# Kernel optimization log

Measured on AMD Instinct MI355X. Metric: run time of the kernel, lower is better.

## Reference

```python
import jax, jax.numpy as jnp
import numpy as np
jax.config.update('jax_enable_x64', True)

B, S, D, H, V, P = 4, 2048, 512, 8, 100000, 256
NGRAMS = list(range(3, 9))  # n-gram lengths 3..8
DH = D // H
SCALE = np.float32(DH ** -0.5)

def _layernorm(x, g, b, eps=1e-5):
    m = jnp.mean(x, -1, keepdims=True)
    v = jnp.mean(jnp.square(x - m), -1, keepdims=True)
    return g * (x - m) / jnp.sqrt(v + eps) + b

def _mha(q, k, v, Wq, bq, Wk, bk, Wv, bv, Wo, bo):
    Bq, Lq, _ = q.shape
    qh = (q @ Wq + bq).reshape(Bq, Lq, H, DH)
    kh = (k @ Wk + bk).reshape(Bq, -1, H, DH)
    vh = (v @ Wv + bv).reshape(Bq, -1, H, DH)
    s = jnp.einsum('bqhd,bkhd->bhqk', qh, kh) * SCALE
    a = jax.nn.softmax(s, axis=-1)
    o = jnp.einsum('bhqk,bkhd->bqhd', a, vh).reshape(Bq, Lq, D)
    return o @ Wo + bo

def _ngram_hash(bytes_seq, n):
    # hash[:, i] = sum_k bytes[:, i-n+1+k] * 256**k for i >= n-1 else 0, then mod V
    # (int64 wraparound for n=8 matches torch semantics)
    b = bytes_seq.astype(jnp.int64)
    h = jnp.zeros_like(b)
    for k in range(n):
        shift = n - 1 - k
        shifted = jnp.pad(b, ((0, 0), (shift, 0)))[:, :S]
        h = h + shifted * (256 ** k)
    h = jnp.where(jnp.arange(S) >= (n - 1), h, 0)
    return h % V

def _forward(bytes_seq, patch_idx, byte_emb, ngram_emb, sWq, sbq, sWk, sbk, sWv, sbv, sWo, sbo, ln1g, ln1b, W1, b1, W2, b2, ln2g, ln2b, cWq, cbq, cWk, cbk, cWv, cbv, cWo, cbo):
    embeds = byte_emb[bytes_seq]  # [B,S,D]
    for j, n in enumerate(NGRAMS):
        embeds = embeds + ngram_emb[j][_ngram_hash(bytes_seq, n)]
    embeds = embeds / np.float32(len(NGRAMS) + 1)
    # one post-norm transformer encoder layer (relu FFN, eval mode / no dropout)
    x = _layernorm(embeds + _mha(embeds, embeds, embeds, sWq, sbq, sWk, sbk, sWv, sbv, sWo, sbo), ln1g, ln1b)
    ff = jax.nn.relu(x @ W1 + b1) @ W2 + b2
    x = _layernorm(x + ff, ln2g, ln2b)
    # gather patch-boundary queries per batch, cross-attend to full sequence
    q = jnp.take_along_axis(x, patch_idx[..., None], axis=1)  # [B,P,D]
    return _mha(q, x, x, cWq, cbq, cWk, cbk, cWv, cbv, cWo, cbo)

def setup_inputs():
    key = jax.random.key(0)
    ks = jax.random.split(key, 20)
    f32 = jnp.float32
    def rn(k, shape, scale=0.02):
        return (jax.random.normal(k, shape, f32) * scale).astype(f32)
    return {
        'bytes_seq': jax.random.randint(ks[0], (B, S), 0, 256, dtype=jnp.int64),
        'patch_idx': jnp.sort(jax.random.randint(ks[1], (B, P), 0, S, dtype=jnp.int64), axis=1),
        'byte_emb': rn(ks[2], (256, D)),
        'ngram_emb': rn(ks[3], (len(NGRAMS), V, D)),
        'sWq': rn(ks[4], (D, D)), 'sbq': jnp.zeros((D,), f32),
        'sWk': rn(ks[5], (D, D)), 'sbk': jnp.zeros((D,), f32),
        'sWv': rn(ks[6], (D, D)), 'sbv': jnp.zeros((D,), f32),
        'sWo': rn(ks[7], (D, D)), 'sbo': jnp.zeros((D,), f32),
        'ln1g': jnp.ones((D,), f32), 'ln1b': jnp.zeros((D,), f32),
        'W1': rn(ks[8], (D, 4 * D)), 'b1': jnp.zeros((4 * D,), f32),
        'W2': rn(ks[9], (4 * D, D)), 'b2': jnp.zeros((D,), f32),
        'ln2g': jnp.ones((D,), f32), 'ln2b': jnp.zeros((D,), f32),
        'cWq': rn(ks[10], (D, D)), 'cbq': jnp.zeros((D,), f32),
        'cWk': rn(ks[11], (D, D)), 'cbk': jnp.zeros((D,), f32),
        'cWv': rn(ks[12], (D, D)), 'cbv': jnp.zeros((D,), f32),
        'cWo': rn(ks[13], (D, D)), 'cbo': jnp.zeros((D,), f32),
    }

def reference(bytes_seq, patch_idx, byte_emb, ngram_emb, sWq, sbq, sWk, sbk, sWv, sbv, sWo, sbo, ln1g, ln1b, W1, b1, W2, b2, ln2g, ln2b, cWq, cbq, cWk, cbk, cWv, cbv, cWo, cbo):
    return _forward(bytes_seq, patch_idx, byte_emb, ngram_emb, sWq, sbq, sWk, sbk, sWv, sbv, sWo, sbo, ln1g, ln1b, W1, b1, W2, b2, ln2g, ln2b, cWq, cbq, cWk, cbk, cWv, cbv, cWo, cbo)
```

## Files before the change

kernel.cpp:

```cpp
#include <hip/hip_runtime.h>
#include <stdint.h>

#define B_   4
#define S_   2048
#define D_   512
#define H_   8
#define DH_  64
#define V_   100000
#define P_   256
#define N_   (B_*S_)
#define NP_  (B_*P_)

typedef _Float16 f16;
typedef _Float16 f16x8 __attribute__((ext_vector_type(8)));
typedef float    f32x4 __attribute__((ext_vector_type(4)));
typedef uint32_t u32x4 __attribute__((ext_vector_type(4)));

#define MFMA16(a,b,c) __builtin_amdgcn_mfma_f32_16x16x32_f16((a),(b),(c),0,0,0)
#define GLDS16(gp, lp) __builtin_amdgcn_global_load_lds( \
    (const __attribute__((address_space(1))) void*)(gp), \
    (__attribute__((address_space(3))) void*)(lp), 16, 0, 0)

struct WJobs {
  const float* src[10];
  f16* dst[10];
  int K[10], N[10], tiles[10];
};

__global__ __launch_bounds__(256) void prep_kernel(WJobs jobs,
    const float* __restrict__ sbq, const float* __restrict__ sbk,
    const float* __restrict__ sbv, const float* __restrict__ cbk,
    const float* __restrict__ cbv, float* __restrict__ bqkv,
    float* __restrict__ bckv,
    const int* __restrict__ bytes_seq, const float* __restrict__ byte_emb,
    const float* __restrict__ ngram_emb, f16* __restrict__ out16)
{
  int bid = blockIdx.x;
  if (bid < 10240) {
    const int j = bid >> 10, tile = bid & 1023;
    if (tile >= jobs.tiles[j]) return;
    const int K = jobs.K[j], N = jobs.N[j];
    const int ntiles = N >> 5;
    const int kt = (tile / ntiles) << 5, nt = (tile % ntiles) << 5;
    __shared__ float T[32][33];
    const int t = threadIdx.x;
    const float* src = jobs.src[j];
    #pragma unroll
    for (int p = 0; p < 4; p++) {
      int lin = t + p * 256;
      int rr = lin >> 5, cc = lin & 31;
      T[rr][cc] = src[(size_t)(kt + rr) * N + nt + cc];
    }
    __syncthreads();
    f16* dst = jobs.dst[j];
    #pragma unroll
    for (int p = 0; p < 4; p++) {
      int lin = t + p * 256;
      int rr = lin >> 5, cc = lin & 31;
      dst[(size_t)(nt + rr) * K + kt + cc] = (f16)T[cc][rr];
    }
    return;
  }
  bid -= 10240;
  if (bid < 10) {
    int t = bid * 256 + threadIdx.x;
    if (t < 512)       bqkv[t] = sbq[t];
    else if (t < 1024) bqkv[t] = sbk[t - 512];
    else if (t < 1536) bqkv[t] = sbv[t - 1024];
    else if (t < 2048) bckv[t - 1536] = cbk[t - 1536];
    else if (t < 2560) bckv[t - 1536] = cbv[t - 2048];
    return;
  }
  bid -= 10;
  const int pos = bid * 2 + (threadIdx.x >> 7);
  const int b = pos / S_, s = pos % S_;
  const int* bs = bytes_seq + (size_t)b * S_;

  int w[8];
  #pragma unroll
  for (int k = 0; k < 8; k++) {
    int p = s - 7 + k;
    w[k] = (p >= 0) ? bs[p] : 0;
  }
  int idx[6];
  #pragma unroll
  for (int j = 0; j < 6; j++) {
    const int n = j + 3;
    int id = 0;
    if (s >= n - 1) {
      uint64_t h = 0;
      for (int k = 0; k < n; k++)
        h += (uint64_t)(uint32_t)w[8 - n + k] << (8 * k);
      long long sh = (long long)h;
      long long r = sh % (long long)V_;
      if (r < 0) r += V_;
      id = (int)r;
    }
    idx[j] = id;
  }
  const int d = (threadIdx.x & 127) * 4;
  float4 acc = *(const float4*)(byte_emb + (size_t)bs[s] * D_ + d);
  #pragma unroll
  for (int j = 0; j < 6; j++) {
    const float4 v = *(const float4*)(ngram_emb + ((size_t)j * V_ + idx[j]) * D_ + d);
    acc.x += v.x; acc.y += v.y; acc.z += v.z; acc.w += v.w;
  }
  const float inv7 = 1.0f / 7.0f;
  f16 t4[4];
  t4[0] = (f16)(acc.x * inv7); t4[1] = (f16)(acc.y * inv7);
  t4[2] = (f16)(acc.z * inv7); t4[3] = (f16)(acc.w * inv7);
  *(uint2*)(out16 + (size_t)pos * D_ + d) = *(uint2*)t4;
}

template<typename OutT, int RELU, int BN, int VTSTART, int K>
__device__ __forceinline__ void gemm_body(
    const f16* __restrict__ A, const f16* __restrict__ Bt,
    const float* __restrict__ bias, OutT* __restrict__ C,
    int N, const int* __restrict__ rowmap,
    f16* __restrict__ vt, int bmi, int bni)
{
  constexpr int NF = BN / 32;
  constexpr int NT = K / 32;
  __shared__ __align__(16) f16 As[2][128 * 32];
  __shared__ __align__(16) f16 Bs[2][BN * 32];
  const int tid = threadIdx.x;
  const int l = tid & 63;
  const int lo4 = l & 15, hi2 = l >> 4;
  const int w = tid >> 6;
  const int wr = w >> 1, wc = w & 1;
  const int bm = bmi * 128, bn = bni * BN;

  const f16* ap[2];
  #pragma unroll
  for (int i = 0; i < 2; i++) {
    int r = bm + i * 64 + (tid >> 2);
    int ar = rowmap ? ((r >> 8) * S_ + rowmap[r]) : r;
    ap[i] = A + (size_t)ar * K + (tid & 3) * 8;
  }
  const f16* bp[BN / 64];
  #pragma unroll
  for (int i = 0; i < BN / 64; i++) {
    int c = i * 256 + tid;
    bp[i] = Bt + (size_t)(bn + (c >> 2)) * K + (c & 3) * 8;
  }

  f32x4 acc[4][NF];
  #pragma unroll
  for (int m = 0; m < 4; m++)
    #pragma unroll
    for (int n = 0; n < NF; n++) acc[m][n] = (f32x4){0.f, 0.f, 0.f, 0.f};

  #pragma unroll
  for (int i = 0; i < 2; i++)
    GLDS16(ap[i], &As[0][(i * 256 + tid) * 8]);
  #pragma unroll
  for (int i = 0; i < BN / 64; i++)
    GLDS16(bp[i], &Bs[0][(i * 256 + tid) * 8]);

  for (int to = 0; to < NT / 8; to++) {
    #pragma unroll
    for (int ti = 0; ti < 8; ti++) {
      const int t = to * 8 + ti;
      __syncthreads();
      const int cur = t & 1;
      if (t + 1 < NT) {
        const int k0 = (t + 1) << 5;
        #pragma unroll
        for (int i = 0; i < 2; i++)
          GLDS16(ap[i] + k0, &As[cur ^ 1][(i * 256 + tid) * 8]);
        #pragma unroll
        for (int i = 0; i < BN / 64; i++)
          GLDS16(bp[i] + k0, &Bs[cur ^ 1][(i * 256 + tid) * 8]);
      }
      f16x8 af[4], bf[NF];
      const f16* pa = &As[cur][(wr * 64 + lo4) * 32 + hi2 * 8];
      const f16* pb = &Bs[cur][(wc * (BN / 2) + lo4) * 32 + hi2 * 8];
      #pragma unroll
      for (int m = 0; m < 4; m++) af[m] = *(const f16x8*)(pa + m * 16 * 32);
      #pragma unroll
      for (int n = 0; n < NF; n++) bf[n] = *(const f16x8*)(pb + n * 16 * 32);
      #pragma unroll
      for (int m = 0; m < 4; m++)
        #pragma unroll
        for (int n = 0; n < NF; n++)
          acc[m][n] = MFMA16(af[m], bf[n], acc[m][n]);
    }
  }

  if constexpr (VTSTART >= 0) {
    if (bn >= VTSTART) {
      #pragma unroll
      for (int n = 0; n < NF; n++) {
        const int col = bn + wc * (BN / 2) + n * 16 + lo4;
        const float bcol = bias[col];
        const int dcol = col - VTSTART;
        const size_t vbase = ((size_t)(dcol >> 6) * 64 + (dcol & 63)) << 11;
        #pragma unroll
        for (int m = 0; m < 4; m++) {
          const int row0 = bm + wr * 64 + m * 16 + hi2 * 4;
          f16 t4[4];
          #pragma unroll
          for (int j = 0; j < 4; j++) t4[j] = (f16)(acc[m][n][j] + bcol);
          *(uint2*)(vt + (((size_t)(row0 >> 11) * 8) << 17) + vbase + (row0 & 2047)) = *(uint2*)t4;
        }
      }
      return;
    }
  }

  #pragma unroll
  for (int n = 0; n < NF; n++) {
    const int col = bn + wc * (BN / 2) + n * 16 + lo4;
    const float bcol = bias[col];
    #pragma unroll
    for (int m = 0; m < 4; m++) {
      const int row0 = bm + wr * 64 + m * 16 + hi2 * 4;
      #pragma unroll
      for (int j = 0; j < 4; j++) {
        float v = acc[m][n][j] + bcol;
        if (RELU) v = fmaxf(v, 0.f);
        C[(size_t)(row0 + j) * N + col] = (OutT)v;
      }
    }
  }
}

template<typename OutT, int RELU, int BN, int VTSTART, int K>
__global__ __launch_bounds__(256) void gemm_f16(
    const f16* __restrict__ A, const f16* __restrict__ Bt,
    const float* __restrict__ bias, OutT* __restrict__ C,
    int N, const int* __restrict__ rowmap, f16* __restrict__ vt)
{
  gemm_body<OutT, RELU, BN, VTSTART, K>(A, Bt, bias, C, N, rowmap, vt,
                                        blockIdx.x, blockIdx.y);
}

__global__ __launch_bounds__(256) void ckv_cq_kernel(
    const f16* __restrict__ X, const f16* __restrict__ CKVT,
    const float* __restrict__ bckv, f16* __restrict__ CKV,
    f16* __restrict__ vt2, const f16* __restrict__ cWqT,
    const float* __restrict__ cbq, f16* __restrict__ CQ,
    const int* __restrict__ pidx)
{
  int bid = blockIdx.x;
  if (bid < 512) {
    gemm_body<f16, 0, 128, 512, 512>(X, CKVT, bckv, CKV, 1024,
                                     nullptr, vt2, bid >> 3, bid & 7);
  } else {
    bid -= 512;
    gemm_body<f16, 0, 64, -1, 512>(X, cWqT, cbq, CQ, 512,
                                   pidx, nullptr, bid >> 3, bid & 7);
  }
}

template<int QG, int CHUNKS>
__global__ __launch_bounds__(256) void attn_f16(
    const f16* __restrict__ Q, int qs,
    const f16* __restrict__ Kp, int kvs,
    const f16* __restrict__ VT, f16* __restrict__ O,
    float* __restrict__ Opart, float* __restrict__ Lpart, int NQ)
{
  constexpr int CL = S_ / CHUNKS;
  constexpr int NT = CL / 64;
  __shared__ __align__(16) f16 Ks[2][64][76];
  __shared__ __align__(16) f16 VtL[2][64 * 64];

  const int tid = threadIdx.x;
  const int w = tid >> 6, l = tid & 63;
  const int lo4 = l & 15, hi2 = l >> 4;
  const int lin = (CHUNKS == 1) ? blockIdx.x : (blockIdx.x & 127);
  const int c   = (CHUNKS == 1) ? 0 : (int)(blockIdx.x >> 7);
  const int h = lin & 7, b = (lin >> 3) & 3, qt = lin >> 5;

  const f16 qscale = (f16)0.18033688f;
  f16x8 qf[QG][2];
  #pragma unroll
  for (int qg = 0; qg < QG; qg++) {
    const int qrow = qt * (64 * QG) + w * (16 * QG) + qg * 16 + lo4;
    const f16* Qp = Q + (size_t)(b * NQ + qrow) * qs + h * DH_ + hi2 * 8;
    qf[qg][0] = *(const f16x8*)(Qp);
    qf[qg][1] = *(const f16x8*)(Qp + 32);
    #pragma unroll
    for (int i = 0; i < 8; i++) { qf[qg][0][i] *= qscale; qf[qg][1][i] *= qscale; }
  }

  const int g2 = lo4 >> 2, j4 = lo4 & 3;
  const int kvp0 = 8 * g2 + j4;
  const int kvp1 = 8 * (g2 ^ 2) + 4 + j4;
  const int pidx = (l ^ 32) << 2;
  const int vswz = lo4 & 7;

  const f16* Kb = Kp + ((size_t)b * S_ + c * CL) * kvs + h * DH_;
  const f16* VTbh = VT + (((size_t)(b * 8 + h)) << 17) + c * CL;

  float lsum[QG];
  f32x4 oacc[QG][4];
  #pragma unroll
  for (int qg = 0; qg < QG; qg++) {
    lsum[qg] = 0.f;
    #pragma unroll
    for (int df = 0; df < 4; df++) oacc[qg][df] = (f32x4){0.f, 0.f, 0.f, 0.f};
  }

  const int r0 = tid >> 3;
  const int c8 = tid & 7;

  #pragma unroll
  for (int i = 0; i < 2; i++) {
    int r = i * 32 + r0;
    GLDS16(VTbh + (size_t)r * 2048 + ((c8 ^ (r & 7)) * 8), &VtL[0][(i * 256 + tid) * 8]);
  }
  f16x8 kreg[2];
  #pragma unroll
  for (int i = 0; i < 2; i++)
    kreg[i] = *(const f16x8*)(Kb + (size_t)(i * 32 + r0) * kvs + c8 * 8);
  #pragma unroll
  for (int i = 0; i < 2; i++)
    *(f16x8*)(&Ks[0][i * 32 + r0][c8 * 8]) = kreg[i];
  __syncthreads();

  int cur = 0;
  for (int t = 0; t < NT; t++) {
    if (t + 1 < NT) {
      const int kt2 = (t + 1) * 64;
      #pragma unroll
      for (int i = 0; i < 2; i++) {
        int r = i * 32 + r0;
        GLDS16(VTbh + (size_t)r * 2048 + kt2 + ((c8 ^ (r & 7)) * 8),
               &VtL[cur ^ 1][(i * 256 + tid) * 8]);
      }
      #pragma unroll
      for (int i = 0; i < 2; i++)
        kreg[i] = *(const f16x8*)(Kb + (size_t)(kt2 + i * 32 + r0) * kvs + c8 * 8);
    }
    f32x4 sacc[QG][4];
    #pragma unroll
    for (int nf = 0; nf < 4; nf++) {
      const int krow = ((nf & 1) ? kvp1 : kvp0) + (nf >> 1) * 32;
      f16x8 kf0 = *(const f16x8*)(&Ks[cur][krow][hi2 * 8]);
      f16x8 kf1 = *(const f16x8*)(&Ks[cur][krow][32 + hi2 * 8]);
      #pragma unroll
      for (int qg = 0; qg < QG; qg++) {
        f32x4 s = (f32x4){0.f, 0.f, 0.f, 0.f};
        s = MFMA16(kf0, qf[qg][0], s);
        s = MFMA16(kf1, qf[qg][1], s);
        sacc[qg][nf] = s;
      }
    }
    uint32_t packs[QG][4][2];
    #pragma unroll
    for (int qg = 0; qg < QG; qg++)
      #pragma unroll
      for (int nf = 0; nf < 4; nf++) {
        float p0 = exp2f(sacc[qg][nf][0]);
        float p1 = exp2f(sacc[qg][nf][1]);
        float p2 = exp2f(sacc[qg][nf][2]);
        float p3 = exp2f(sacc[qg][nf][3]);
        lsum[qg] += (p0 + p1) + (p2 + p3);
        packs[qg][nf][0] = __builtin_bit_cast(uint32_t, __builtin_amdgcn_cvt_pkrtz(p0, p1));
        packs[qg][nf][1] = __builtin_bit_cast(uint32_t, __builtin_amdgcn_cvt_pkrtz(p2, p3));
      }
    #pragma unroll
    for (int ks = 0; ks < 2; ks++) {
      f16x8 pb[QG];
      #pragma unroll
      for (int qg = 0; qg < QG; qg++) {
        uint32_t w0 = packs[qg][2 * ks][0];
        uint32_t w1 = packs[qg][2 * ks][1];
        uint32_t w2 = (uint32_t)__builtin_amdgcn_ds_bpermute(pidx, (int)packs[qg][2 * ks + 1][0]);
        uint32_t w3 = (uint32_t)__builtin_amdgcn_ds_bpermute(pidx, (int)packs[qg][2 * ks + 1][1]);
        u32x4 bw = (u32x4){w0, w1, w2, w3};
        pb[qg] = __builtin_bit_cast(f16x8, bw);
      }
      #pragma unroll
      for (int df = 0; df < 4; df++) {
        const int r = df * 16 + lo4;
        const int cc = (ks * 4 + hi2) ^ vswz;
        f16x8 vf = *(const f16x8*)(&VtL[cur][r * 64 + cc * 8]);
        #pragma unroll
        for (int qg = 0; qg < QG; qg++)
          oacc[qg][df] = MFMA16(vf, pb[qg], oacc[qg][df]);
      }
    }
    if (t + 1 < NT) {
      #pragma unroll
      for (int i = 0; i < 2; i++)
        *(f16x8*)(&Ks[cur ^ 1][i * 32 + r0][c8 * 8]) = kreg[i];
    }
    __syncthreads();
    cur ^= 1;
  }

  #pragma unroll
  for (int qg = 0; qg < QG; qg++) {
    float r = lsum[qg];
    r += __shfl_xor(r, 16, 64);
    r += __shfl_xor(r, 32, 64);
    const int orow = qt * (64 * QG) + w * (16 * QG) + qg * 16 + lo4;
    if constexpr (CHUNKS == 1) {
      const float invl = 1.0f / r;
      f16* Ob = O + (size_t)(b * NQ + orow) * D_ + h * DH_ + hi2 * 4;
      #pragma unroll
      for (int df = 0; df < 4; df++) {
        f16 t4[4];
        #pragma unroll
        for (int j = 0; j < 4; j++) t4[j] = (f16)(oacc[qg][df][j] * invl);
        *(uint2*)(Ob + df * 16) = *(uint2*)t4;
      }
    } else {
      float* Op = Opart + ((size_t)c * NP_ + b * NQ + orow) * D_ + h * DH_ + hi2 * 4;
      #pragma unroll
      for (int df = 0; df < 4; df++) {
        float4 v = {oacc[qg][df][0], oacc[qg][df][1], oacc[qg][df][2], oacc[qg][df][3]};
        *(float4*)(Op + df * 16) = v;
      }
      if (hi2 == 0)
        Lpart[((size_t)c * NP_ + b * NQ + orow) * H_ + h] = r;
    }
  }
}

__global__ __launch_bounds__(128) void attn_reduce(
    const float* __restrict__ Opart, const float* __restrict__ Lpart,
    f16* __restrict__ CO)
{
  const int row = blockIdx.x;
  const int col = threadIdx.x * 4;
  const int h = col >> 6;
  float4 o = {0.f, 0.f, 0.f, 0.f};
  float ls = 0.f;
  #pragma unroll
  for (int c = 0; c < 4; c++) {
    const float4 v = *(const float4*)(Opart + ((size_t)c * NP_ + row) * D_ + col);
    o.x += v.x; o.y += v.y; o.z += v.z; o.w += v.w;
    ls += Lpart[((size_t)c * NP_ + row) * H_ + h];
  }
  const float inv = 1.0f / ls;
  f16 t4[4];
  t4[0] = (f16)(o.x * inv); t4[1] = (f16)(o.y * inv);
  t4[2] = (f16)(o.z * inv); t4[3] = (f16)(o.w * inv);
  *(uint2*)(CO + (size_t)row * D_ + col) = *(uint2*)t4;
}

__global__ __launch_bounds__(256) void ln_kernel(
    const f16* __restrict__ a, const f16* __restrict__ r,
    const float* __restrict__ g, const float* __restrict__ be,
    f16* __restrict__ out)
{
  const int row = blockIdx.x * 2 + (threadIdx.x >> 7);
  const int t = threadIdx.x & 127;
  const f16* ap = a + (size_t)row * D_ + t * 4;
  const f16* rp = r + (size_t)row * D_ + t * 4;
  uint2 au = *(const uint2*)ap, ru = *(const uint2*)rp;
  f16 a4[4], r4[4];
  *(uint2*)a4 = au; *(uint2*)r4 = ru;
  float x0 = (float)a4[0] + (float)r4[0];
  float x1 = (float)a4[1] + (float)r4[1];
  float x2 = (float)a4[2] + (float)r4[2];
  float x3 = (float)a4[3] + (float)r4[3];
  float sm = x0 + x1 + x2 + x3;
  float sq = x0*x0 + x1*x1 + x2*x2 + x3*x3;
  #pragma unroll
  for (int off = 32; off > 0; off >>= 1) {
    sm += __shfl_down(sm, off, 64);
    sq += __shfl_down(sq, off, 64);
  }
  __shared__ float s0[4], s1[4];
  if ((threadIdx.x & 63) == 0) { s0[threadIdx.x >> 6] = sm; s1[threadIdx.x >> 6] = sq; }
  __syncthreads();
  const int base = (threadIdx.x >> 7) * 2;
  const float Sm = s0[base] + s0[base + 1];
  const float Sq = s1[base] + s1[base + 1];
  const float mean = Sm * (1.0f / 512.0f);
  const float var  = Sq * (1.0f / 512.0f) - mean * mean;
  const float inv  = rsqrtf(var + 1e-5f);
  const float4 vg = *(const float4*)(g + t * 4);
  const float4 vb = *(const float4*)(be + t * 4);
  f16 o4[4];
  o4[0] = (f16)(vg.x * (x0 - mean) * inv + vb.x);
  o4[1] = (f16)(vg.y * (x1 - mean) * inv + vb.y);
  o4[2] = (f16)(vg.z * (x2 - mean) * inv + vb.z);
  o4[3] = (f16)(vg.w * (x3 - mean) * inv + vb.w);
  *(uint2*)(out + (size_t)row * D_ + t * 4) = *(uint2*)o4;
}

extern "C" void kernel_launch(void* const* d_in, const int* in_sizes, int n_in,
                              void* d_out, int out_size, void* d_ws, size_t ws_size,
                              hipStream_t stream) {
  const int*   bytes_seq = (const int*)  d_in[0];
  const int*   patch_idx = (const int*)  d_in[1];
  const float* byte_emb  = (const float*)d_in[2];
  const float* ngram_emb = (const float*)d_in[3];
  const float* sWq = (const float*)d_in[4];  const float* sbq = (const float*)d_in[5];
  const float* sWk = (const float*)d_in[6];  const float* sbk = (const float*)d_in[7];
  const float* sWv = (const float*)d_in[8];  const float* sbv = (const float*)d_in[9];
  const float* sWo = (const float*)d_in[10]; const float* sbo = (const float*)d_in[11];
  const float* ln1g = (const float*)d_in[12]; const float* ln1b = (const float*)d_in[13];
  const float* W1 = (const float*)d_in[14];  const float* b1 = (const float*)d_in[15];
  const float* W2 = (const float*)d_in[16];  const float* b2 = (const float*)d_in[17];
  const float* ln2g = (const float*)d_in[18]; const float* ln2b = (const float*)d_in[19];
  const float* cWq = (const float*)d_in[20]; const float* cbq = (const float*)d_in[21];
  const float* cWk = (const float*)d_in[22]; const float* cbk = (const float*)d_in[23];
  const float* cWv = (const float*)d_in[24]; const float* cbv = (const float*)d_in[25];
  const float* cWo = (const float*)d_in[26]; const float* cbo = (const float*)d_in[27];

  char* base = (char*)d_ws;
  const size_t MB = 1u << 20;
  f16* E16     = (f16*)(base + 0 * MB);
  f16* TMP16   = (f16*)(base + 8 * MB);
  f16* X116    = (f16*)(base + 16 * MB);
  f16* X216    = (f16*)(base + 24 * MB);
  f16* QKV16   = (f16*)(base + 32 * MB);
  f16* AT16    = (f16*)(base + 56 * MB);
  f16* HID16   = (f16*)(base + 64 * MB);
  f16* CKV16   = (f16*)(base + 96 * MB);
  f16* CQ16    = (f16*)(base + 112 * MB);
  f16* CO16    = (f16*)(base + 113 * MB);
  f16* WT      = (f16*)(base + 114 * MB);
  float* bqkv  = (float*)(base + 123 * MB);
  float* bckv  = bqkv + 1536;
  f16* VT      = (f16*)(base + 124 * MB);
  f16* VT2     = (f16*)(base + 132 * MB);
  float* OPART = (float*)(base + 140 * MB);
  float* LPART = (float*)(base + 148 * MB);

  f16* QKVT = WT;
  f16* sWoT = QKVT + 786432;
  f16* W1T  = sWoT + 262144;
  f16* W2T  = W1T + 1048576;
  f16* cWqT = W2T + 1048576;
  f16* CKVT = cWqT + 262144;
  f16* cWoT = CKVT + 524288;

  WJobs wj;
  {
    const float* wsrc[10] = {sWq, sWk, sWv, sWo, W1, W2, cWq, cWk, cWv, cWo};
    f16* wdst[10] = {QKVT, QKVT + 262144, QKVT + 524288, sWoT, W1T, W2T,
                     cWqT, CKVT, CKVT + 262144, cWoT};
    const int wK[10] = {512,512,512,512, 512,2048, 512,512,512,512};
    const int wN[10] = {512,512,512,512, 2048,512, 512,512,512,512};
    for (int i = 0; i < 10; i++) {
      wj.src[i] = wsrc[i]; wj.dst[i] = wdst[i];
      wj.K[i] = wK[i]; wj.N[i] = wN[i];
      wj.tiles[i] = (wK[i] >> 5) * (wN[i] >> 5);
    }
  }

  const dim3 blk256(256), blk128(128);

  prep_kernel<<<10240 + 10 + 4096, blk256, 0, stream>>>(
      wj, sbq, sbk, sbv, cbk, cbv, bqkv, bckv,
      bytes_seq, byte_emb, ngram_emb, E16);

  gemm_f16<f16, 0, 128, 1024, 512><<<dim3(64, 12), blk256, 0, stream>>>(
      E16, QKVT, bqkv, QKV16, 1536, nullptr, VT);

  attn_f16<2, 1><<<512, blk256, 0, stream>>>(
      QKV16, 1536, QKV16 + 512, 1536, VT, AT16, nullptr, nullptr, S_);

  gemm_f16<f16, 0, 64, -1, 512><<<dim3(64, 8), blk256, 0, stream>>>(
      AT16, sWoT, sbo, TMP16, 512, nullptr, nullptr);
  ln_kernel<<<N_/2, blk256, 0, stream>>>(E16, TMP16, ln1g, ln1b, X116);

  gemm_f16<f16, 1, 128, -1, 512><<<dim3(64, 16), blk256, 0, stream>>>(
      X116, W1T, b1, HID16, 2048, nullptr, nullptr);
  gemm_f16<f16, 0, 64, -1, 2048><<<dim3(64, 8), blk256, 0, stream>>>(
      HID16, W2T, b2, TMP16, 512, nullptr, nullptr);
  ln_kernel<<<N_/2, blk256, 0, stream>>>(X116, TMP16, ln2g, ln2b, X216);

  ckv_cq_kernel<<<576, blk256, 0, stream>>>(
      X216, CKVT, bckv, CKV16, VT2, cWqT, cbq, CQ16, patch_idx);
  attn_f16<1, 4><<<512, blk256, 0, stream>>>(
      CQ16, 512, CKV16, 1024, VT2, nullptr, OPART, LPART, P_);
  attn_reduce<<<NP_, blk128, 0, stream>>>(OPART, LPART, CO16);

  gemm_f16<float, 0, 64, -1, 512><<<dim3(8, 8), blk256, 0, stream>>>(
      CO16, cWoT, cbo, (float*)d_out, 512, nullptr, nullptr);
}
```

Baseline: 278.9 us.

## Split-K the final cross-attention output projection and vectorize GEMM epilogue stores

The final 1024x512x512 output projection, which launched only 64 blocks, becomes a 4-way split-K GEMM (256 blocks) writing fp32 partials into the reused OPART buffer, followed by a small reduce kernel that adds the bias. The GEMM body gains lda/ldb parameters for the strided K slices. It also swaps the MFMA operand order so each lane holds four consecutive columns, which allows vectorized float4/uint2 epilogue stores and a vector bias load. The cost is an extra launch plus partial-buffer traffic, and the V-transpose store path now writes scalar halves instead of packed stores.

```diff
diff --git a/kernel.cpp b/kernel.cpp
--- a/kernel.cpp
+++ b/kernel.cpp
@@ -117,10 +117,11 @@
     const f16* __restrict__ A, const f16* __restrict__ Bt,
     const float* __restrict__ bias, OutT* __restrict__ C,
     int N, const int* __restrict__ rowmap,
-    f16* __restrict__ vt, int bmi, int bni)
+    f16* __restrict__ vt, int bmi, int bni, int lda, int ldb)
 {
   constexpr int NF = BN / 32;
   constexpr int NT = K / 32;
+  constexpr int U  = (NT < 8) ? NT : 8;
   __shared__ __align__(16) f16 As[2][128 * 32];
   __shared__ __align__(16) f16 Bs[2][BN * 32];
   const int tid = threadIdx.x;
@@ -135,13 +136,13 @@
   for (int i = 0; i < 2; i++) {
     int r = bm + i * 64 + (tid >> 2);
     int ar = rowmap ? ((r >> 8) * S_ + rowmap[r]) : r;
-    ap[i] = A + (size_t)ar * K + (tid & 3) * 8;
+    ap[i] = A + (size_t)ar * lda + (tid & 3) * 8;
   }
   const f16* bp[BN / 64];
   #pragma unroll
   for (int i = 0; i < BN / 64; i++) {
     int c = i * 256 + tid;
-    bp[i] = Bt + (size_t)(bn + (c >> 2)) * K + (c & 3) * 8;
+    bp[i] = Bt + (size_t)(bn + (c >> 2)) * ldb + (tid & 3) * 8;
   }
 
   f32x4 acc[4][NF];
@@ -157,10 +158,10 @@
   for (int i = 0; i < BN / 64; i++)
     GLDS16(bp[i], &Bs[0][(i * 256 + tid) * 8]);
 
-  for (int to = 0; to < NT / 8; to++) {
-    #pragma unroll
-    for (int ti = 0; ti < 8; ti++) {
-      const int t = to * 8 + ti;
+  for (int to = 0; to < NT / U; to++) {
+    #pragma unroll
+    for (int ti = 0; ti < U; ti++) {
+      const int t = to * U + ti;
       __syncthreads();
       const int cur = t & 1;
       if (t + 1 < NT) {
@@ -183,7 +184,7 @@
       for (int m = 0; m < 4; m++)
         #pragma unroll
         for (int n = 0; n < NF; n++)
-          acc[m][n] = MFMA16(af[m], bf[n], acc[m][n]);
+          acc[m][n] = MFMA16(bf[n], af[m], acc[m][n]);
     }
   }
 
@@ -191,17 +192,19 @@
     if (bn >= VTSTART) {
       #pragma unroll
       for (int n = 0; n < NF; n++) {
-        const int col = bn + wc * (BN / 2) + n * 16 + lo4;
-        const float bcol = bias[col];
-        const int dcol = col - VTSTART;
-        const size_t vbase = ((size_t)(dcol >> 6) * 64 + (dcol & 63)) << 11;
+        const int col0 = bn + wc * (BN / 2) + n * 16 + hi2 * 4;
+        float bb[4] = {0.f, 0.f, 0.f, 0.f};
+        if (bias) *(float4*)bb = *(const float4*)(bias + col0);
         #pragma unroll
         for (int m = 0; m < 4; m++) {
-          const int row0 = bm + wr * 64 + m * 16 + hi2 * 4;
-          f16 t4[4];
+          const int s = bm + wr * 64 + m * 16 + lo4;
           #pragma unroll
-          for (int j = 0; j < 4; j++) t4[j] = (f16)(acc[m][n][j] + bcol);
-          *(uint2*)(vt + (((size_t)(row0 >> 11) * 8) << 17) + vbase + (row0 & 2047)) = *(uint2*)t4;
+          for (int j = 0; j < 4; j++) {
+            const int dcol = col0 + j - VTSTART;
+            vt[(((size_t)(s >> 11) * 8 + (dcol >> 6)) << 17) +
+               ((size_t)(dcol & 63) << 11) + (s & 2047)] =
+                (f16)(acc[m][n][j] + bb[j]);
+          }
         }
       }
       return;
@@ -210,16 +213,26 @@
 
   #pragma unroll
   for (int n = 0; n < NF; n++) {
-    const int col = bn + wc * (BN / 2) + n * 16 + lo4;
-    const float bcol = bias[col];
+    const int col0 = bn + wc * (BN / 2) + n * 16 + hi2 * 4;
+    float bb[4] = {0.f, 0.f, 0.f, 0.f};
+    if (bias) *(float4*)bb = *(const float4*)(bias + col0);
     #pragma unroll
     for (int m = 0; m < 4; m++) {
-      const int row0 = bm + wr * 64 + m * 16 + hi2 * 4;
+      const int row = bm + wr * 64 + m * 16 + lo4;
+      float v[4];
       #pragma unroll
       for (int j = 0; j < 4; j++) {
-        float v = acc[m][n][j] + bcol;
-        if (RELU) v = fmaxf(v, 0.f);
-        C[(size_t)(row0 + j) * N + col] = (OutT)v;
+        v[j] = acc[m][n][j] + bb[j];
+        if (RELU) v[j] = fmaxf(v[j], 0.f);
+      }
+      if constexpr (sizeof(OutT) == 2) {
+        f16 t4[4];
+        #pragma unroll
+        for (int j = 0; j < 4; j++) t4[j] = (f16)v[j];
+        *(uint2*)((f16*)C + (size_t)row * N + col0) = *(uint2*)t4;
+      } else {
+        float4 t4 = {v[0], v[1], v[2], v[3]};
+        *(float4*)((float*)C + (size_t)row * N + col0) = t4;
       }
     }
   }
@@ -232,7 +245,7 @@
     int N, const int* __restrict__ rowmap, f16* __restrict__ vt)
 {
   gemm_body<OutT, RELU, BN, VTSTART, K>(A, Bt, bias, C, N, rowmap, vt,
-                                        blockIdx.x, blockIdx.y);
+                                        blockIdx.x, blockIdx.y, K, K);
 }
 
 __global__ __launch_bounds__(256) void ckv_cq_kernel(
@@ -245,12 +258,37 @@
   int bid = blockIdx.x;
   if (bid < 512) {
     gemm_body<f16, 0, 128, 512, 512>(X, CKVT, bckv, CKV, 1024,
-                                     nullptr, vt2, bid >> 3, bid & 7);
+                                     nullptr, vt2, bid >> 3, bid & 7, 512, 512);
   } else {
     bid -= 512;
     gemm_body<f16, 0, 64, -1, 512>(X, cWqT, cbq, CQ, 512,
-                                   pidx, nullptr, bid >> 3, bid & 7);
-  }
+                                   pidx, nullptr, bid >> 3, bid & 7, 512, 512);
+  }
+}
+
+__global__ __launch_bounds__(256) void co_splitk(
+    const f16* __restrict__ A, const f16* __restrict__ Bt,
+    float* __restrict__ part)
+{
+  const int z = blockIdx.z;
+  gemm_body<float, 0, 64, -1, 128>(A + z * 128, Bt + z * 128, nullptr,
+      part + (size_t)z * NP_ * 512, 512, nullptr, nullptr,
+      blockIdx.x, blockIdx.y, 512, 512);
+}
+
+__global__ __launch_bounds__(128) void co_reduce(
+    const float* __restrict__ part, const float* __restrict__ bias,
+    float* __restrict__ out)
+{
+  const int row = blockIdx.x;
+  const int col = threadIdx.x * 4;
+  float4 s = *(const float4*)(bias + col);
+  #pragma unroll
+  for (int c = 0; c < 4; c++) {
+    const float4 v = *(const float4*)(part + ((size_t)c * NP_ + row) * 512 + col);
+    s.x += v.x; s.y += v.y; s.z += v.z; s.w += v.w;
+  }
+  *(float4*)(out + (size_t)row * 512 + col) = s;
 }
 
 template<int QG, int CHUNKS>
@@ -574,6 +612,6 @@
       CQ16, 512, CKV16, 1024, VT2, nullptr, OPART, LPART, P_);
   attn_reduce<<<NP_, blk128, 0, stream>>>(OPART, LPART, CO16);
 
-  gemm_f16<float, 0, 64, -1, 512><<<dim3(8, 8), blk256, 0, stream>>>(
-      CO16, cWoT, cbo, (float*)d_out, 512, nullptr, nullptr);
-}
+  co_splitk<<<dim3(8, 8, 4), blk256, 0, stream>>>(CO16, cWoT, OPART);
+  co_reduce<<<NP_, blk128, 0, stream>>>(OPART, cbo, (float*)d_out);
+}
```

Measured after the change: 277.3 us. About the same (-0.6%).
